# Performance work log

Hardware: AMD Instinct MI355X
Metric: run time of the kernel (lower is better)

Reference implementation:

```python
import jax, jax.numpy as jnp
import numpy as np

P = 3  # spline degree in both u and v (init_kwargs degrees=[3,3])


def _knot_vector(n_cp, p):
    # clamped uniform knot vector, length n_cp+p+1 (matches calculate_knot_vectors)
    kv = np.concatenate([np.zeros(p), np.linspace(0.0, 1.0, n_cp - p + 1), np.ones(p)])
    return jnp.asarray(kv.astype(np.float32))


def _basis_and_deriv(u, spans, knots, p):
    # Cox-de Boor basis functions and 1st derivatives (NURBS Book A2.3), vectorized
    # u, spans: [S,F,E]; knots: 1D. Returns (N, dN) each [S,F,E,p+1].
    left = [None] * (p + 1)
    right = [None] * (p + 1)
    ndu = [[None] * (p + 1) for _ in range(p + 1)]
    ndu[0][0] = jnp.ones_like(u)
    for j in range(1, p + 1):
        left[j] = u - knots[spans - j + 1]
        right[j] = knots[spans + j] - u
        saved = jnp.zeros_like(u)
        for r in range(j):
            ndu[j][r] = right[r + 1] + left[j - r]  # knot differences
            tmp = ndu[r][j - 1] / ndu[j][r]
            ndu[r][j] = saved + right[r + 1] * tmp
            saved = left[j - r] * tmp
        ndu[j][j] = saved
    n = 1  # nth_derivative = 1
    ders = [[jnp.zeros_like(u) for _ in range(p + 1)] for _ in range(n + 1)]
    for j in range(p + 1):
        ders[0][j] = ndu[j][p]
    for r in range(p + 1):
        a = [[jnp.zeros_like(u) for _ in range(p + 1)] for _ in range(2)]
        a[0][0] = jnp.ones_like(u)
        s1, s2 = 0, 1
        for k in range(1, n + 1):
            d = jnp.zeros_like(u)
            rk, pk = r - k, p - k
            if r >= k:
                a[s2][0] = a[s1][0] / ndu[pk + 1][rk]
                d = a[s2][0] * ndu[rk][pk]
            j1 = 1 if rk >= -1 else -rk
            j2 = k - 1 if r - 1 <= pk else p - r
            for jj in range(j1, j2 + 1):
                a[s2][jj] = (a[s1][jj] - a[s1][jj - 1]) / ndu[pk + 1][rk + jj]
                d = d + a[s2][jj] * ndu[rk + jj][pk]
            if r <= pk:
                a[s2][k] = -a[s1][k - 1] / ndu[pk + 1][r]
                d = d + a[s2][k] * ndu[r][pk]
            ders[k][r] = d
            s1, s2 = s2, s1
    # multiply by p!/(p-k)! factor for k=1
    N0 = jnp.stack(ders[0], axis=-1)
    N1 = jnp.stack([ders[1][j] * p for j in range(p + 1)], axis=-1)
    return N0, N1


def _forward(evaluation_points, control_points):
    S, F, n_u, n_v, _ = control_points.shape
    p = P
    knots_u = _knot_vector(n_u, p)
    knots_v = _knot_vector(n_v, p)
    u = evaluation_points[..., 0]
    v = evaluation_points[..., 1]
    # uniform knot span search: floor(t * n_intervals) + degree (find_spans, uniform branch)
    spans_u = jnp.clip(jnp.floor(u * (n_u - p)).astype(jnp.int32) + p, p, n_u - 1)
    spans_v = jnp.clip(jnp.floor(v * (n_v - p)).astype(jnp.int32) + p, p, n_v - 1)
    bu0, bu1 = _basis_and_deriv(u, spans_u, knots_u, p)  # [S,F,E,p+1]
    bv0, bv1 = _basis_and_deriv(v, spans_v, knots_v, p)
    offs = jnp.arange(p + 1)
    iu = spans_u[..., None] - p + offs  # [S,F,E,p+1] control indices in u
    iv = spans_v[..., None] - p + offs
    sidx = jnp.arange(S)[:, None, None, None, None]
    fidx = jnp.arange(F)[None, :, None, None, None]
    # gather local (p+1)x(p+1) control net per eval point: [S,F,E,p+1,p+1,3]
    g = control_points[sidx, fidx, iu[..., :, None], iv[..., None, :]]
    pts = jnp.einsum('sfeijc,sfei,sfej->sfec', g, bu0, bv0)
    du = jnp.einsum('sfeijc,sfei,sfej->sfec', g, bu1, bv0)
    dv = jnp.einsum('sfeijc,sfei,sfej->sfec', g, bu0, bv1)
    nrm = jnp.cross(du, dv)
    nrm = nrm / (jnp.linalg.norm(nrm, axis=-1, keepdims=True) + 1e-12)
    ones = jnp.ones_like(pts[..., :1])
    points4 = jnp.concatenate([pts, ones], axis=-1)
    normals4 = jnp.concatenate([nrm, jnp.zeros_like(ones)], axis=-1)
    return points4, normals4


def setup_inputs() -> dict:
    key = jax.random.key(0)
    k1, k2 = jax.random.split(key)
    S, F, E = 4, 4, 65536
    N_CP = 32
    evaluation_points = jax.random.uniform(k1, (S, F, E, 2), dtype=jnp.float32)
    control_points = jax.random.normal(k2, (S, F, N_CP, N_CP, 3), dtype=jnp.float32)
    return {"evaluation_points": evaluation_points, "control_points": control_points}


def reference(evaluation_points, control_points):
    return _forward(evaluation_points, control_points)
```

## Files before the change

### kernel.cpp

```cpp
#include <hip/hip_runtime.h>

typedef __fp16 half2_t __attribute__((ext_vector_type(2)));
typedef float f32x4 __attribute__((ext_vector_type(4)));

#define S_DIM 4
#define F_DIM 4
#define E_DIM 65536
#define NCP   32

union H2U { unsigned u; half2_t h; };

__device__ __forceinline__ unsigned pkh(float a, float b) {
    H2U c; c.h.x = (__fp16)a; c.h.y = (__fp16)b;
    return c.u;
}
__device__ __forceinline__ half2_t ash2(unsigned u) {
    H2U c; c.u = u;
    return c.h;
}
__device__ __forceinline__ half2_t mkw(float a, float b) {
    half2_t h; h.x = (__fp16)a; h.y = (__fp16)b;
    return h;
}

__device__ __forceinline__ void basis3(float u, float fs, float* N0, float* N1) {
    const float h = 1.0f / 29.0f;
    const float b = fs * h;
    const float L1 = u - b;
    const float L2 = u - fmaxf(b - h, 0.0f);
    const float L3 = u - fmaxf(b - 2.0f * h, 0.0f);
    const float R1 = (b + h) - u;
    const float R2 = fminf(b + 2.0f * h, 1.0f) - u;
    const float R3 = fminf(b + 3.0f * h, 1.0f) - u;
    const float i10 = __builtin_amdgcn_rcpf(R1 + L1);
    const float v01 = R1 * i10;
    const float v11 = L1 * i10;
    const float i20 = __builtin_amdgcn_rcpf(R1 + L2);
    float t = v01 * i20;
    const float v02 = R1 * t;
    float s = L2 * t;
    const float i21 = __builtin_amdgcn_rcpf(R2 + L1);
    t = v11 * i21;
    const float v12 = s + R2 * t;
    const float v22 = L1 * t;
    const float i30 = __builtin_amdgcn_rcpf(R1 + L3);
    t = v02 * i30;
    N0[0] = R1 * t;
    s = L3 * t;
    const float i31 = __builtin_amdgcn_rcpf(R2 + L2);
    t = v12 * i31;
    N0[1] = s + R2 * t;
    s = L2 * t;
    const float i32 = __builtin_amdgcn_rcpf(R3 + L1);
    t = v22 * i32;
    N0[2] = s + R3 * t;
    N0[3] = L1 * t;
    const float a0 = v02 * i30, a1 = v12 * i31, a2 = v22 * i32;
    N1[0] = -3.0f * a0;
    N1[1] = 3.0f * (a0 - a1);
    N1[2] = 3.0f * (a1 - a2);
    N1[3] = 3.0f * a2;
}

__global__ __launch_bounds__(256, 6) void nurbs_eval_kernel(
    const float* __restrict__ ep,
    const float* __restrict__ cp,
    float* __restrict__ out)
{
    __shared__ unsigned sm[3 * 32 * 33];

    const int sf  = blockIdx.y;
    const int tid = threadIdx.x;

    const int e   = blockIdx.x * 256 + tid;
    const int idx = sf * E_DIM + e;
    const float2 uvp = ((const float2*)ep)[idx];

    const int su_ = tid >> 3, sm_ = tid & 7;
    const float* rowp = cp + ((size_t)sf * 1024 + (size_t)su_ * 32) * 3;
    const int o = 12 * sm_;
    const float4 Ld0 = *(const float4*)(rowp + o);
    const float4 Ld1 = *(const float4*)(rowp + o + 4);
    const float4 Ld2 = *(const float4*)(rowp + o + 8);
    const float4 Ld3 = *(const float4*)(rowp + ((sm_ == 7) ? 80 : (o + 12)));

    const float uu = uvp.x, vv = uvp.y;

    const float fsu = fminf(fmaxf(floorf(uu * 29.0f), 0.0f), 28.0f);
    const float fsv = fminf(fmaxf(floorf(vv * 29.0f), 0.0f), 28.0f);
    const int bu = (int)fsu, bv = (int)fsv;

    float bu0[4], bu1[4], bv0[4], bv1[4];
    basis3(uu, fsu, bu0, bu1);
    basis3(vv, fsv, bv0, bv1);

    const half2_t w00 = mkw(bv0[0], bv0[1]);
    const half2_t w01 = mkw(bv0[2], bv0[3]);
    const half2_t w10 = mkw(bv1[0], bv1[1]);
    const half2_t w11 = mkw(bv1[2], bv1[3]);

    {
        float f[16];
        f[0]=Ld0.x; f[1]=Ld0.y; f[2]=Ld0.z; f[3]=Ld0.w;
        f[4]=Ld1.x; f[5]=Ld1.y; f[6]=Ld1.z; f[7]=Ld1.w;
        f[8]=Ld2.x; f[9]=Ld2.y; f[10]=Ld2.z; f[11]=Ld2.w;
        f[12]=Ld3.x; f[13]=Ld3.y; f[14]=Ld3.z; f[15]=Ld3.w;
        unsigned* E0w = sm;
        unsigned* E1w = sm + 1056;
        unsigned* E2w = sm + 2112;
#pragma unroll
        for (int ee = 0; ee < 4; ++ee) {
            const int v = 4 * sm_ + ee;
            const int a = su_ * 33 + v;
            E0w[a] = pkh(f[3*ee+0], f[3*ee+3]);
            E1w[a] = pkh(f[3*ee+1], f[3*ee+4]);
            E2w[a] = pkh(f[3*ee+2], f[3*ee+5]);
        }
    }
    __syncthreads();

    const unsigned* E0 = sm;
    const unsigned* E1 = sm + 1056;
    const unsigned* E2 = sm + 2112;
    const int base = 33 * bu + bv;

    float px=0.f, py=0.f, pz=0.f;
    float dux=0.f, duy=0.f, duz=0.f;
    float dvx=0.f, dvy=0.f, dvz=0.f;

#pragma unroll
    for (int i = 0; i < 4; ++i) {
        const int a = base + 33 * i;
        const half2_t x0 = ash2(E0[a]), x1 = ash2(E0[a + 2]);
        const half2_t y0 = ash2(E1[a]), y1 = ash2(E1[a + 2]);
        const half2_t z0 = ash2(E2[a]), z1 = ash2(E2[a + 2]);
        const float t0x = __builtin_amdgcn_fdot2(x1, w01, __builtin_amdgcn_fdot2(x0, w00, 0.0f, false), false);
        const float t1x = __builtin_amdgcn_fdot2(x1, w11, __builtin_amdgcn_fdot2(x0, w10, 0.0f, false), false);
        const float t0y = __builtin_amdgcn_fdot2(y1, w01, __builtin_amdgcn_fdot2(y0, w00, 0.0f, false), false);
        const float t1y = __builtin_amdgcn_fdot2(y1, w11, __builtin_amdgcn_fdot2(y0, w10, 0.0f, false), false);
        const float t0z = __builtin_amdgcn_fdot2(z1, w01, __builtin_amdgcn_fdot2(z0, w00, 0.0f, false), false);
        const float t1z = __builtin_amdgcn_fdot2(z1, w11, __builtin_amdgcn_fdot2(z0, w10, 0.0f, false), false);
        px  = fmaf(bu0[i], t0x, px);  py  = fmaf(bu0[i], t0y, py);  pz  = fmaf(bu0[i], t0z, pz);
        dux = fmaf(bu1[i], t0x, dux); duy = fmaf(bu1[i], t0y, duy); duz = fmaf(bu1[i], t0z, duz);
        dvx = fmaf(bu0[i], t1x, dvx); dvy = fmaf(bu0[i], t1y, dvy); dvz = fmaf(bu0[i], t1z, dvz);
    }

    float nx = duy * dvz - duz * dvy;
    float ny = duz * dvx - dux * dvz;
    float nz = dux * dvy - duy * dvx;
    float n2 = nx * nx + ny * ny + nz * nz;
    const float du2 = dux*dux + duy*duy + duz*duz;
    const float dv2 = dvx*dvx + dvy*dvy + dvz*dvz;

    if (n2 < 4e-3f * (du2 * dv2)) {
        float fu0[4], fu1[4], fv0[4], fv1[4];
        basis3(uu, (float)bu, fu0, fu1);
        basis3(vv, (float)bv, fv0, fv1);
        const float* patch = cp + (size_t)sf * 3072;
        float DUX=0.f, DUY=0.f, DUZ=0.f, DVX=0.f, DVY=0.f, DVZ=0.f;
#pragma unroll
        for (int i = 0; i < 4; ++i) {
            float s0x=0.f, s0y=0.f, s0z=0.f, s1x=0.f, s1y=0.f, s1z=0.f;
#pragma unroll
            for (int j = 0; j < 4; ++j) {
                const float* p = patch + (((bu + i) * 32) + (bv + j)) * 3;
                const float gx = p[0], gy = p[1], gz = p[2];
                s0x = fmaf(gx, fv0[j], s0x); s0y = fmaf(gy, fv0[j], s0y); s0z = fmaf(gz, fv0[j], s0z);
                s1x = fmaf(gx, fv1[j], s1x); s1y = fmaf(gy, fv1[j], s1y); s1z = fmaf(gz, fv1[j], s1z);
            }
            DUX = fmaf(fu1[i], s0x, DUX); DUY = fmaf(fu1[i], s0y, DUY); DUZ = fmaf(fu1[i], s0z, DUZ);
            DVX = fmaf(fu0[i], s1x, DVX); DVY = fmaf(fu0[i], s1y, DVY); DVZ = fmaf(fu0[i], s1z, DVZ);
        }
        nx = DUY * DVZ - DUZ * DVY;
        ny = DUZ * DVX - DUX * DVZ;
        nz = DUX * DVY - DUY * DVX;
        n2 = nx * nx + ny * ny + nz * nz;
    }

    const float inv = __builtin_amdgcn_rsqf(fmaxf(n2, 1e-24f));
    nx *= inv; ny *= inv; nz *= inv;

    f32x4* outv = (f32x4*)out;
    f32x4 pt; pt[0]=px; pt[1]=py; pt[2]=pz; pt[3]=1.0f;
    f32x4 nm; nm[0]=nx; nm[1]=ny; nm[2]=nz; nm[3]=0.0f;
    __builtin_nontemporal_store(pt, &outv[idx]);
    __builtin_nontemporal_store(nm, &outv[(size_t)S_DIM * F_DIM * E_DIM + idx]);
}

extern "C" void kernel_launch(void* const* d_in, const int* in_sizes, int n_in,
                              void* d_out, int out_size, void* d_ws, size_t ws_size,
                              hipStream_t stream) {
    const float* ep = (const float*)d_in[0];
    const float* cp = (const float*)d_in[1];
    float* out = (float*)d_out;

    dim3 grid(E_DIM / 256, S_DIM * F_DIM);
    dim3 block(256);
    hipLaunchKernelGGL(nurbs_eval_kernel, grid, block, 0, stream, ep, cp, out);
}
```

Measured before the change: 19.50 us.

## Defer rare fp32 normal fallback to a separate worklist fixup kernel

Result: slower. 39.94 us (+104.8%).

```diff
diff --git a/kernel.cpp b/kernel.cpp
--- a/kernel.cpp
+++ b/kernel.cpp
@@ -65,7 +65,9 @@
 __global__ __launch_bounds__(256, 6) void nurbs_eval_kernel(
     const float* __restrict__ ep,
     const float* __restrict__ cp,
-    float* __restrict__ out)
+    float* __restrict__ out,
+    unsigned* __restrict__ wsc,
+    unsigned cap)
 {
     __shared__ unsigned sm[3 * 32 * 33];
 
@@ -148,33 +150,13 @@
     float nx = duy * dvz - duz * dvy;
     float ny = duz * dvx - dux * dvz;
     float nz = dux * dvy - duy * dvx;
-    float n2 = nx * nx + ny * ny + nz * nz;
+    const float n2 = nx * nx + ny * ny + nz * nz;
     const float du2 = dux*dux + duy*duy + duz*duz;
     const float dv2 = dvx*dvx + dvy*dvy + dvz*dvz;
 
     if (n2 < 4e-3f * (du2 * dv2)) {
-        float fu0[4], fu1[4], fv0[4], fv1[4];
-        basis3(uu, (float)bu, fu0, fu1);
-        basis3(vv, (float)bv, fv0, fv1);
-        const float* patch = cp + (size_t)sf * 3072;
-        float DUX=0.f, DUY=0.f, DUZ=0.f, DVX=0.f, DVY=0.f, DVZ=0.f;
-#pragma unroll
-        for (int i = 0; i < 4; ++i) {
-            float s0x=0.f, s0y=0.f, s0z=0.f, s1x=0.f, s1y=0.f, s1z=0.f;
-#pragma unroll
-            for (int j = 0; j < 4; ++j) {
-                const float* p = patch + (((bu + i) * 32) + (bv + j)) * 3;
-                const float gx = p[0], gy = p[1], gz = p[2];
-                s0x = fmaf(gx, fv0[j], s0x); s0y = fmaf(gy, fv0[j], s0y); s0z = fmaf(gz, fv0[j], s0z);
-                s1x = fmaf(gx, fv1[j], s1x); s1y = fmaf(gy, fv1[j], s1y); s1z = fmaf(gz, fv1[j], s1z);
-            }
-            DUX = fmaf(fu1[i], s0x, DUX); DUY = fmaf(fu1[i], s0y, DUY); DUZ = fmaf(fu1[i], s0z, DUZ);
-            DVX = fmaf(fu0[i], s1x, DVX); DVY = fmaf(fu0[i], s1y, DVY); DVZ = fmaf(fu0[i], s1z, DVZ);
-        }
-        nx = DUY * DVZ - DUZ * DVY;
-        ny = DUZ * DVX - DUX * DVZ;
-        nz = DUX * DVY - DUY * DVX;
-        n2 = nx * nx + ny * ny + nz * nz;
+        const unsigned pos = atomicAdd(wsc, 1u);
+        if (pos < cap) wsc[1 + pos] = (unsigned)idx;
     }
 
     const float inv = __builtin_amdgcn_rsqf(fmaxf(n2, 1e-24f));
@@ -185,6 +167,50 @@
     f32x4 nm; nm[0]=nx; nm[1]=ny; nm[2]=nz; nm[3]=0.0f;
     __builtin_nontemporal_store(pt, &outv[idx]);
     __builtin_nontemporal_store(nm, &outv[(size_t)S_DIM * F_DIM * E_DIM + idx]);
+}
+
+__global__ __launch_bounds__(256) void nurbs_fixup_kernel(
+    const float* __restrict__ ep,
+    const float* __restrict__ cp,
+    float* __restrict__ out,
+    const unsigned* __restrict__ wsc,
+    unsigned cap)
+{
+    const unsigned count = min(wsc[0], cap);
+    for (unsigned i = blockIdx.x * 256 + threadIdx.x; i < count; i += 16 * 256) {
+        const int idx = (int)wsc[1 + i];
+        const int sf = idx >> 16;
+        const float2 uvp = ((const float2*)ep)[idx];
+        const float uu = uvp.x, vv = uvp.y;
+        const float fsu = fminf(fmaxf(floorf(uu * 29.0f), 0.0f), 28.0f);
+        const float fsv = fminf(fmaxf(floorf(vv * 29.0f), 0.0f), 28.0f);
+        const int bu = (int)fsu, bv = (int)fsv;
+        float fu0[4], fu1[4], fv0[4], fv1[4];
+        basis3(uu, fsu, fu0, fu1);
+        basis3(vv, fsv, fv0, fv1);
+        const float* patch = cp + (size_t)sf * 3072;
+        float DUX=0.f, DUY=0.f, DUZ=0.f, DVX=0.f, DVY=0.f, DVZ=0.f;
+#pragma unroll
+        for (int r = 0; r < 4; ++r) {
+            float s0x=0.f, s0y=0.f, s0z=0.f, s1x=0.f, s1y=0.f, s1z=0.f;
+#pragma unroll
+            for (int j = 0; j < 4; ++j) {
+                const float* p = patch + (((bu + r) * 32) + (bv + j)) * 3;
+                const float gx = p[0], gy = p[1], gz = p[2];
+                s0x = fmaf(gx, fv0[j], s0x); s0y = fmaf(gy, fv0[j], s0y); s0z = fmaf(gz, fv0[j], s0z);
+                s1x = fmaf(gx, fv1[j], s1x); s1y = fmaf(gy, fv1[j], s1y); s1z = fmaf(gz, fv1[j], s1z);
+            }
+            DUX = fmaf(fu1[r], s0x, DUX); DUY = fmaf(fu1[r], s0y, DUY); DUZ = fmaf(fu1[r], s0z, DUZ);
+            DVX = fmaf(fu0[r], s1x, DVX); DVY = fmaf(fu0[r], s1y, DVY); DVZ = fmaf(fu0[r], s1z, DVZ);
+        }
+        float nx = DUY * DVZ - DUZ * DVY;
+        float ny = DUZ * DVX - DUX * DVZ;
+        float nz = DUX * DVY - DUY * DVX;
+        const float n2 = nx * nx + ny * ny + nz * nz;
+        const float inv = __builtin_amdgcn_rsqf(fmaxf(n2, 1e-24f));
+        f32x4 nm; nm[0]=nx*inv; nm[1]=ny*inv; nm[2]=nz*inv; nm[3]=0.0f;
+        ((f32x4*)out)[(size_t)S_DIM * F_DIM * E_DIM + idx] = nm;
+    }
 }
 
 extern "C" void kernel_launch(void* const* d_in, const int* in_sizes, int n_in,
@@ -193,8 +219,17 @@
     const float* ep = (const float*)d_in[0];
     const float* cp = (const float*)d_in[1];
     float* out = (float*)d_out;
+    unsigned* wsc = (unsigned*)d_ws;
+
+    unsigned cap = 0;
+    if (ws_size >= 8) {
+        size_t c = ws_size / 4 - 1;
+        cap = (unsigned)(c > 1048576 ? 1048576 : c);
+    }
+    hipMemsetAsync(d_ws, 0, 4, stream);
 
     dim3 grid(E_DIM / 256, S_DIM * F_DIM);
     dim3 block(256);
-    hipLaunchKernelGGL(nurbs_eval_kernel, grid, block, 0, stream, ep, cp, out);
-}
+    hipLaunchKernelGGL(nurbs_eval_kernel, grid, block, 0, stream, ep, cp, out, wsc, cap);
+    hipLaunchKernelGGL(nurbs_fixup_kernel, dim3(16), block, 0, stream, ep, cp, out, wsc, cap);
+}
```
